# Performance work log

Hardware: AMD Instinct MI355X
Metric: run time of the kernel (lower is better)

Reference implementation:

```python
import jax, jax.numpy as jnp
import numpy as np

N, E, G = 50000, 800000, 64
IN_C, HID, HEADS, OUT_C = 128, 64, 4, 10
NEG_SLOPE = 0.2
EPS = 1e-16


def gat_conv(x, src, dst, W, a_src, a_dst, bias, heads, out_ch):
    # x: [N, F_in]; W: [F_in, heads*out_ch]; a_*: [heads, out_ch]; bias: [heads*out_ch]
    n = x.shape[0]
    h = (x @ W).reshape(n, heads, out_ch)                     # [N, H, C]
    alpha_src = jnp.einsum('nhc,hc->nh', h, a_src)            # [N, H]
    alpha_dst = jnp.einsum('nhc,hc->nh', h, a_dst)            # [N, H]
    e = jax.nn.leaky_relu(alpha_src[src] + alpha_dst[dst], NEG_SLOPE)  # [E, H]
    # segment softmax over incoming edges of each destination node
    m = jax.ops.segment_max(e, dst, num_segments=n)
    ex = jnp.exp(e - m[dst])
    denom = jax.ops.segment_sum(ex, dst, num_segments=n)
    alpha = ex / (denom[dst] + EPS)                           # [E, H]
    msg = h[src] * alpha[:, :, None]                          # [E, H, C]
    out = jax.ops.segment_sum(msg, dst, num_segments=n)       # [N, H, C]
    return out.reshape(n, heads * out_ch) + bias


def setup_inputs() -> dict:
    key = jax.random.key(0)
    ks = jax.random.split(key, 16)
    s = 0.1
    inp = {
        'x': jax.random.normal(ks[0], (N, IN_C), dtype=jnp.float32),
        'edge_index': jax.random.randint(ks[1], (2, E), 0, N, dtype=jnp.int64)
            if jax.config.jax_enable_x64 else jax.random.randint(ks[1], (2, E), 0, N).astype(jnp.int32),
        'batch': jnp.sort(jax.random.randint(ks[2], (N,), 0, G).astype(jnp.int32)),
        'W1': s * jax.random.normal(ks[3], (IN_C, HEADS * HID), dtype=jnp.float32),
        'as1': s * jax.random.normal(ks[4], (HEADS, HID), dtype=jnp.float32),
        'ad1': s * jax.random.normal(ks[5], (HEADS, HID), dtype=jnp.float32),
        'b1': jnp.zeros((HEADS * HID,), jnp.float32),
        'W2': s * jax.random.normal(ks[6], (HEADS * HID, HEADS * HID), dtype=jnp.float32),
        'as2': s * jax.random.normal(ks[7], (HEADS, HID), dtype=jnp.float32),
        'ad2': s * jax.random.normal(ks[8], (HEADS, HID), dtype=jnp.float32),
        'b2': jnp.zeros((HEADS * HID,), jnp.float32),
        'W3': s * jax.random.normal(ks[9], (HEADS * HID, HID), dtype=jnp.float32),
        'as3': s * jax.random.normal(ks[10], (1, HID), dtype=jnp.float32),
        'ad3': s * jax.random.normal(ks[11], (1, HID), dtype=jnp.float32),
        'b3': jnp.zeros((HID,), jnp.float32),
        'Wc': s * jax.random.normal(ks[12], (HID, OUT_C), dtype=jnp.float32),
        'bc': jnp.zeros((OUT_C,), jnp.float32),
    }
    return inp


def reference(x, edge_index, batch, W1, as1, ad1, b1, W2, as2, ad2, b2,
              W3, as3, ad3, b3, Wc, bc):
    n = x.shape[0]
    loop = jnp.arange(n, dtype=edge_index.dtype)
    src = jnp.concatenate([edge_index[0], loop])  # add self-loops (PyG default)
    dst = jnp.concatenate([edge_index[1], loop])

    h = gat_conv(x, src, dst, W1, as1, ad1, b1, HEADS, HID)
    h = jax.nn.elu(h)
    h = gat_conv(h, src, dst, W2, as2, ad2, b2, HEADS, HID)
    h = jax.nn.elu(h)
    h = gat_conv(h, src, dst, W3, as3, ad3, b3, 1, HID)

    # global mean pool over graphs
    sums = jax.ops.segment_sum(h, batch, num_segments=G)            # [G, HID]
    counts = jax.ops.segment_sum(jnp.ones((n,), h.dtype), batch, num_segments=G)
    pooled = sums / jnp.maximum(counts, 1.0)[:, None]

    logits = pooled @ Wc + bc                                       # [G, OUT_C]
    return logits
```

## Files before the change

kernel.cpp:

```cpp
#include <hip/hip_runtime.h>

#define NEG_SLOPE 0.2f
#define EPSV 1e-16f

typedef unsigned short ushort_t;
typedef unsigned char uchar_t;
typedef __attribute__((ext_vector_type(8))) short bf16x8;
typedef __attribute__((ext_vector_type(4))) float f32x4;
typedef __attribute__((ext_vector_type(2))) float f32x2;

__device__ __forceinline__ ushort_t f2bf(float f) {
    union { float f; unsigned u; } v; v.f = f;
    unsigned r = v.u + 0x7FFFu + ((v.u >> 16) & 1u);
    return (ushort_t)(r >> 16);
}
__device__ __forceinline__ float bf2f(ushort_t u) {
    union { unsigned u; float f; } v; v.u = ((unsigned)u) << 16;
    return v.f;
}
__device__ __forceinline__ uchar_t f2fp8(float f) {
    int p = __builtin_amdgcn_cvt_pk_fp8_f32(f, 0.f, 0, false);
    return (uchar_t)(p & 0xff);
}

__global__ __launch_bounds__(256)
void count_kernel(const int* __restrict__ ei, int* __restrict__ deg, int E, int n) {
    int i = blockIdx.x * blockDim.x + threadIdx.x;
    int M = E + n;
    if (i >= M) return;
    int d = (i < E) ? ei[E + i] : (i - E);
    atomicAdd(&deg[d], 1);
}

__global__ __launch_bounds__(1024)
void scan1_kernel(const int* __restrict__ deg, int* __restrict__ indptr,
                  int* __restrict__ bsum, int n) {
    __shared__ int wsum[16];
    const int t = threadIdx.x;
    const int lane = t & 63;
    const int w = t >> 6;
    const int i = blockIdx.x * 1024 + t;
    int v = (i < n) ? deg[i] : 0;
    int s = v;
    #pragma unroll
    for (int off = 1; off < 64; off <<= 1) {
        int u = __shfl_up(s, off);
        if (lane >= off) s += u;
    }
    if (lane == 63) wsum[w] = s;
    __syncthreads();
    if (t < 16) {
        int ws_ = wsum[t];
        #pragma unroll
        for (int off = 1; off < 16; off <<= 1) {
            int u = __shfl_up(ws_, off);
            if (t >= off) ws_ += u;
        }
        wsum[t] = ws_;
    }
    __syncthreads();
    int woff = (w > 0) ? wsum[w - 1] : 0;
    if (i < n) indptr[i + 1] = woff + s;
    if (t == 0) bsum[blockIdx.x] = wsum[15];
}

__global__ __launch_bounds__(1024)
void scan3_kernel(int* __restrict__ indptr, int* __restrict__ cursor,
                  const int* __restrict__ bsum, int nb, int n) {
    __shared__ int boff_s;
    const int t = threadIdx.x;
    if (t < 64) {
        int v = (t < nb) ? bsum[t] : 0;
        int s = v;
        #pragma unroll
        for (int off = 1; off < 64; off <<= 1) {
            int u = __shfl_up(s, off);
            if (t >= off) s += u;
        }
        if (t == (int)blockIdx.x) boff_s = s - v;
    }
    __syncthreads();
    const int boff = boff_s;
    int i = blockIdx.x * 1024 + t;
    if (i < n) {
        int val = indptr[i + 1] + boff;
        indptr[i + 1] = val;
        cursor[i + 1] = val;
    }
    if (i == 0) { indptr[0] = 0; cursor[0] = 0; }
}

__global__ __launch_bounds__(256)
void scatter_kernel(const int* __restrict__ ei, int* __restrict__ cursor,
                    int* __restrict__ csr_src, int E, int n) {
    int i = blockIdx.x * blockDim.x + threadIdx.x;
    int M = E + n;
    if (i >= M) return;
    int s, d;
    if (i < E) { s = ei[i]; d = ei[E + i]; }
    else       { s = i - E; d = i - E; }
    int pos = atomicAdd(&cursor[d], 1);
    csr_src[pos] = s;
}

__global__ __launch_bounds__(256)
void prep_kernel(const float* __restrict__ x, ushort_t* __restrict__ xb, int nx4,
                 const float* __restrict__ W1, ushort_t* __restrict__ Wt1,
                 const float* __restrict__ W2, ushort_t* __restrict__ Wt2,
                 const float* __restrict__ W3, ushort_t* __restrict__ Wt3,
                 int K1, int* __restrict__ deg, int n) {
    long idx = (long)blockIdx.x * 256 + threadIdx.x;
    if (idx < nx4) {
        float4 v = *reinterpret_cast<const float4*>(&x[idx * 4]);
        ushort4 o;
        o.x = f2bf(v.x); o.y = f2bf(v.y); o.z = f2bf(v.z); o.w = f2bf(v.w);
        *reinterpret_cast<ushort4*>(&xb[idx * 4]) = o;
        return;
    }
    idx -= nx4;
    if (idx < (long)K1 * 256) {
        int c = (int)(idx % 256), k = (int)(idx / 256);
        Wt1[(long)c * K1 + k] = f2bf(W1[idx]);
        return;
    }
    idx -= (long)K1 * 256;
    if (idx < 256 * 256) {
        int c = (int)(idx % 256), k = (int)(idx / 256);
        Wt2[(long)c * 256 + k] = f2bf(W2[idx]);
        return;
    }
    idx -= 256 * 256;
    if (idx < 256 * 64) {
        int c = (int)(idx % 64), k = (int)(idx / 64);
        Wt3[(long)c * 256 + k] = f2bf(W3[idx]);
        return;
    }
    idx -= 256 * 64;
    if (idx < n) deg[idx] = 0;
}

template<int NC>
__global__ __launch_bounds__(256)
void mfma_gemm_alpha_kernel(const ushort_t* __restrict__ A, const ushort_t* __restrict__ Wt,
                            uchar_t* __restrict__ C,
                            const float* __restrict__ a_src, const float* __restrict__ a_dst,
                            float* __restrict__ asrc, float* __restrict__ adst,
                            int M, int K, int N, int H) {
    constexpr int TBN = NC * 64;
    constexpr int MI  = (NC == 2) ? 4 : 2;
    __shared__ ushort_t As[128][40];
    __shared__ ushort_t Ws[TBN][40];
    const int tid  = threadIdx.x;
    const int w    = tid >> 6;
    const int lane = tid & 63;
    const int l15  = lane & 15;
    const int l4   = lane >> 4;
    const int row0 = blockIdx.x * 128;
    const int col0 = blockIdx.y * TBN;
    const int rbase = (NC == 2) ? (w & 1) * 64 : w * 32;
    const int cbase = (NC == 2) ? (w >> 1) * 64 : 0;

    f32x4 acc[MI][4];
    #pragma unroll
    for (int mi = 0; mi < MI; ++mi)
        #pragma unroll
        for (int ni = 0; ni < 4; ++ni)
            acc[mi][ni] = (f32x4){0.f, 0.f, 0.f, 0.f};

    for (int k0 = 0; k0 < K; k0 += 32) {
        #pragma unroll
        for (int it = 0; it < 2; ++it) {
            int idx = tid + it * 256;
            int r = idx >> 2, seg = idx & 3;
            int gr = row0 + r;
            uint4 v = make_uint4(0u, 0u, 0u, 0u);
            if (gr < M)
                v = *reinterpret_cast<const uint4*>(&A[(long)gr * K + k0 + seg * 8]);
            *reinterpret_cast<uint4*>(&As[r][seg * 8]) = v;
        }
        #pragma unroll
        for (int it = 0; it < NC; ++it) {
            int idx = tid + it * 256;
            int r = idx >> 2, seg = idx & 3;
            uint4 v = *reinterpret_cast<const uint4*>(&Wt[(long)(col0 + r) * K + k0 + seg * 8]);
            *reinterpret_cast<uint4*>(&Ws[r][seg * 8]) = v;
        }
        __syncthreads();
        bf16x8 af[MI], bfv[4];
        #pragma unroll
        for (int mi = 0; mi < MI; ++mi)
            af[mi] = *reinterpret_cast<const bf16x8*>(&As[rbase + mi * 16 + l15][8 * l4]);
        #pragma unroll
        for (int ni = 0; ni < 4; ++ni)
            bfv[ni] = *reinterpret_cast<const bf16x8*>(&Ws[cbase + ni * 16 + l15][8 * l4]);
        #pragma unroll
        for (int mi = 0; mi < MI; ++mi)
            #pragma unroll
            for (int ni = 0; ni < 4; ++ni)
                acc[mi][ni] = __builtin_amdgcn_mfma_f32_16x16x32_bf16(
                    af[mi], bfv[ni], acc[mi][ni], 0, 0, 0);
        __syncthreads();
    }

    #pragma unroll
    for (int mi = 0; mi < MI; ++mi)
        #pragma unroll
        for (int reg = 0; reg < 4; ++reg) {
            int gr = row0 + rbase + mi * 16 + l4 * 4 + reg;
            if (gr < M) {
                #pragma unroll
                for (int ni = 0; ni < 4; ++ni)
                    C[(long)gr * N + col0 + cbase + ni * 16 + l15] = f2fp8(acc[mi][ni][reg]);
            }
        }

    const int hd = (col0 + cbase) >> 6;
    float aS[4], aD[4];
    #pragma unroll
    for (int ni = 0; ni < 4; ++ni) {
        aS[ni] = a_src[hd * 64 + ni * 16 + l15];
        aD[ni] = a_dst[hd * 64 + ni * 16 + l15];
    }
    #pragma unroll
    for (int mi = 0; mi < MI; ++mi)
        #pragma unroll
        for (int reg = 0; reg < 4; ++reg) {
            float s = 0.f, d = 0.f;
            #pragma unroll
            for (int ni = 0; ni < 4; ++ni) {
                s += acc[mi][ni][reg] * aS[ni];
                d += acc[mi][ni][reg] * aD[ni];
            }
            #pragma unroll
            for (int off = 1; off < 16; off <<= 1) {
                s += __shfl_xor(s, off);
                d += __shfl_xor(d, off);
            }
            int gr = row0 + rbase + mi * 16 + l4 * 4 + reg;
            if (l15 == 0 && gr < M) {
                asrc[gr * H + hd] = s;
                adst[gr * H + hd] = d;
            }
        }
}

__global__ __launch_bounds__(256)
void aggregate4_kernel(const uchar_t* __restrict__ h, const float* __restrict__ asrc,
                       const float* __restrict__ adst, const int* __restrict__ indptr,
                       const int* __restrict__ csr_src, const float* __restrict__ bias,
                       ushort_t* __restrict__ out, int n, int apply_elu) {
    __shared__ int   sOff[4][64];
    __shared__ float sEx[4][4][68];
    const int node = (blockIdx.x * blockDim.x + threadIdx.x) >> 6;
    const int lane = threadIdx.x & 63;
    const int w    = threadIdx.x >> 6;
    if (node >= n) return;
    const int hd   = lane >> 4;
    const int eidx = lane & 15;
    const int beg = indptr[node], end = indptr[node + 1];
    const float ad = adst[node * 4 + hd];
    const uchar_t* __restrict__ hrow = h + 4 * lane;

    float sum_ex = 0.f;
    float ax = 0.f, ay = 0.f, az = 0.f, aw = 0.f;
    for (int cb = beg; cb < end; cb += 64) {
        const int cnt = min(64, end - cb);
        int s[4];
        float ex[4];
        #pragma unroll
        for (int j = 0; j < 4; ++j) {
            int idx = eidx + 16 * j;
            s[j] = (idx < cnt) ? csr_src[cb + idx] : 0;
        }
        #pragma unroll
        for (int j = 0; j < 4; ++j) {
            float t = asrc[s[j] * 4 + hd] + ad;
            t = t > 0.f ? t : NEG_SLOPE * t;
            ex[j] = (eidx + 16 * j < cnt) ? __expf(t) : 0.f;
        }
        float csum = (ex[0] + ex[1]) + (ex[2] + ex[3]);
        #pragma unroll
        for (int off = 1; off < 16; off <<= 1) csum += __shfl_xor(csum, off);
        sum_ex += csum;
        #pragma unroll
        for (int j = 0; j < 4; ++j) sEx[w][hd][eidx + 16 * j] = ex[j];
        if (hd == 0) {
            #pragma unroll
            for (int j = 0; j < 4; ++j) sOff[w][eidx + 16 * j] = s[j] << 8;
        }
        int i = 0;
        for (; i + 8 <= cnt; i += 8) {
            int o[8];
            float ee[8];
            unsigned v[8];
            #pragma unroll
            for (int u = 0; u < 8; ++u) o[u] = sOff[w][i + u];
            #pragma unroll
            for (int u = 0; u < 8; ++u) v[u] = *reinterpret_cast<const unsigned*>(hrow + o[u]);
            #pragma unroll
            for (int u = 0; u < 8; ++u) ee[u] = sEx[w][hd][i + u];
            #pragma unroll
            for (int u = 0; u < 8; ++u) {
                f32x2 lo = __builtin_amdgcn_cvt_pk_f32_fp8((int)v[u], false);
                f32x2 hi = __builtin_amdgcn_cvt_pk_f32_fp8((int)v[u], true);
                ax += ee[u] * lo[0];
                ay += ee[u] * lo[1];
                az += ee[u] * hi[0];
                aw += ee[u] * hi[1];
            }
        }
        for (; i < cnt; ++i) {
            int o = sOff[w][i];
            float ee = sEx[w][hd][i];
            unsigned v = *reinterpret_cast<const unsigned*>(hrow + o);
            f32x2 lo = __builtin_amdgcn_cvt_pk_f32_fp8((int)v, false);
            f32x2 hi = __builtin_amdgcn_cvt_pk_f32_fp8((int)v, true);
            ax += ee * lo[0]; ay += ee * lo[1];
            az += ee * hi[0]; aw += ee * hi[1];
        }
    }
    const float inv = 1.f / (sum_ex + EPSV);
    float4 b4 = *reinterpret_cast<const float4*>(bias + 4 * lane);
    float ox = ax * inv + b4.x;
    float oy = ay * inv + b4.y;
    float oz = az * inv + b4.z;
    float ow = aw * inv + b4.w;
    if (apply_elu) {
        ox = ox > 0.f ? ox : expm1f(ox);
        oy = oy > 0.f ? oy : expm1f(oy);
        oz = oz > 0.f ? oz : expm1f(oz);
        ow = ow > 0.f ? ow : expm1f(ow);
    }
    ushort4 o4;
    o4.x = f2bf(ox); o4.y = f2bf(oy); o4.z = f2bf(oz); o4.w = f2bf(ow);
    *reinterpret_cast<ushort4*>(out + (long)node * 256 + 4 * lane) = o4;
}

__global__ __launch_bounds__(256)
void aggregate_kernel(const uchar_t* __restrict__ h, const float* __restrict__ asrc,
                      const float* __restrict__ adst, const int* __restrict__ indptr,
                      const int* __restrict__ csr_src, const float* __restrict__ bias,
                      ushort_t* __restrict__ out, int n, int apply_elu) {
    __shared__ int   sInd[4][64];
    __shared__ float sEx[4][64];
    const int node = (blockIdx.x * blockDim.x + threadIdx.x) >> 6;
    const int lane = threadIdx.x & 63;
    const int w    = threadIdx.x >> 6;
    if (node >= n) return;
    const int beg = indptr[node];
    const int end = indptr[node + 1];
    const float ad = adst[node];
    const uchar_t* __restrict__ hh = h + lane;

    float sum_ex = 0.f, acc = 0.f;
    for (int cb = beg; cb < end; cb += 64) {
        const int cnt = min(64, end - cb);
        int s = 0;
        float ex = 0.f;
        if (lane < cnt) {
            s = csr_src[cb + lane];
            float e = asrc[s] + ad;
            e = e > 0.f ? e : NEG_SLOPE * e;
            ex = __expf(e);
        }
        float cs = ex;
        #pragma unroll
        for (int off = 32; off > 0; off >>= 1) cs += __shfl_xor(cs, off);
        sum_ex += cs;
        sInd[w][lane] = s;
        sEx[w][lane]  = ex;
        int i = 0;
        for (; i + 8 <= cnt; i += 8) {
            int si[8];
            float ei_[8], vi[8];
            #pragma unroll
            for (int u = 0; u < 8; ++u) si[u] = sInd[w][i + u];
            #pragma unroll
            for (int u = 0; u < 8; ++u) {
                unsigned b = hh[(long)si[u] * 64];
                f32x2 r = __builtin_amdgcn_cvt_pk_f32_fp8((int)b, false);
                vi[u] = r[0];
            }
            #pragma unroll
            for (int u = 0; u < 8; ++u) ei_[u] = sEx[w][i + u];
            #pragma unroll
            for (int u = 0; u < 8; ++u) acc += ei_[u] * vi[u];
        }
        for (; i < cnt; ++i) {
            unsigned b = hh[(long)sInd[w][i] * 64];
            f32x2 r = __builtin_amdgcn_cvt_pk_f32_fp8((int)b, false);
            acc += sEx[w][i] * r[0];
        }
    }
    float o = acc / (sum_ex + EPSV) + bias[lane];
    if (apply_elu) o = o > 0.f ? o : expm1f(o);
    out[(long)node * 64 + lane] = f2bf(o);
}

constexpr int POOL_CHUNK = 128;

__global__ __launch_bounds__(64)
void pool_kernel(const ushort_t* __restrict__ h, const int* __restrict__ batch,
                 float* __restrict__ sums, int* __restrict__ counts, int n) {
    int lane = threadIdx.x;
    int start = blockIdx.x * POOL_CHUNK;
    if (start >= n) return;
    int end = min(start + POOL_CHUNK, n);
    int gcur = batch[start];
    float acc = 0.f;
    int run = 0;
    for (int i = start; i < end; ++i) {
        int g = batch[i];
        if (g != gcur) {
            atomicAdd(&sums[gcur * 64 + lane], acc);
            if (lane == 0) atomicAdd(&counts[gcur], run);
            acc = 0.f; run = 0; gcur = g;
        }
        acc += bf2f(h[(long)i * 64 + lane]);
        ++run;
    }
    atomicAdd(&sums[gcur * 64 + lane], acc);
    if (lane == 0) atomicAdd(&counts[gcur], run);
}

__global__ void classify_kernel(const float* __restrict__ sums, const int* __restrict__ counts,
                                const float* __restrict__ Wc, const float* __restrict__ bc,
                                float* __restrict__ out, int G) {
    int t = threadIdx.x;
    if (t >= G * 10) return;
    int g = t / 10, o = t - g * 10;
    int c_ = counts[g];
    float inv = 1.f / (float)(c_ > 1 ? c_ : 1);
    float acc = bc[o];
    for (int c = 0; c < 64; ++c)
        acc += sums[g * 64 + c] * inv * Wc[c * 10 + o];
    out[t] = acc;
}

extern "C" void kernel_launch(void* const* d_in, const int* in_sizes, int n_in,
                              void* d_out, int out_size, void* d_ws, size_t ws_size,
                              hipStream_t stream) {
    const float* x   = (const float*)d_in[0];
    const int*   ei  = (const int*)d_in[1];
    const int*   bat = (const int*)d_in[2];
    const float* W1  = (const float*)d_in[3];
    const float* as1 = (const float*)d_in[4];
    const float* ad1 = (const float*)d_in[5];
    const float* b1  = (const float*)d_in[6];
    const float* W2  = (const float*)d_in[7];
    const float* as2 = (const float*)d_in[8];
    const float* ad2 = (const float*)d_in[9];
    const float* b2  = (const float*)d_in[10];
    const float* W3  = (const float*)d_in[11];
    const float* as3 = (const float*)d_in[12];
    const float* ad3 = (const float*)d_in[13];
    const float* b3  = (const float*)d_in[14];
    const float* Wc  = (const float*)d_in[15];
    const float* bc  = (const float*)d_in[16];
    float* out = (float*)d_out;

    const int N = in_sizes[2];
    const int E = in_sizes[1] / 2;
    const int M = E + N;
    const int IN_C = in_sizes[0] / N;
    const int G = out_size / 10;

    char* p = (char*)d_ws;
    auto carve = [&](size_t bytes) -> void* {
        void* r = (void*)p;
        p += (bytes + 255) & ~(size_t)255;
        return r;
    };
    uchar_t*  hA  = (uchar_t*)carve((size_t)N * 256);
    ushort_t* hB  = (ushort_t*)carve((size_t)N * 256 * 2);
    ushort_t* xb  = (ushort_t*)carve((size_t)N * IN_C * 2);
    ushort_t* Wt1 = (ushort_t*)carve((size_t)256 * IN_C * 2);
    ushort_t* Wt2 = (ushort_t*)carve((size_t)256 * 256 * 2);
    ushort_t* Wt3 = (ushort_t*)carve((size_t)64 * 256 * 2);
    float* asrc = (float*)carve((size_t)N * 4 * 4);
    float* adst = (float*)carve((size_t)N * 4 * 4);
    float* sums = (float*)carve((size_t)G * 64 * 4 + (size_t)G * 4);
    int*   cnts = (int*)(sums + (size_t)G * 64);
    int*   deg  = (int*)carve((size_t)N * 4);
    int*   iptr = (int*)carve((size_t)(N + 1) * 4);
    int*   csr  = (int*)carve((size_t)M * 4);
    int*   bsum = (int*)carve(256 * 4);
    (void)ws_size; (void)n_in;

    const int NB = (N + 1023) / 1024;

    {
        long nx4 = (long)N * IN_C / 4;
        long total = nx4 + (long)IN_C * 256 + 256 * 256 + 256 * 64 + N;
        prep_kernel<<<(int)((total + 255) / 256), 256, 0, stream>>>(
            x, xb, (int)nx4, W1, Wt1, W2, Wt2, W3, Wt3, IN_C, deg, N);
    }

    count_kernel<<<(M + 255) / 256, 256, 0, stream>>>(ei, deg, E, N);
    scan1_kernel<<<NB, 1024, 0, stream>>>(deg, iptr, bsum, N);
    scan3_kernel<<<NB, 1024, 0, stream>>>(iptr, deg, bsum, NB, N);
    scatter_kernel<<<(M + 255) / 256, 256, 0, stream>>>(ei, deg, csr, E, N);

    {
        dim3 grid((N + 127) / 128, 2);
        mfma_gemm_alpha_kernel<2><<<grid, 256, 0, stream>>>(xb, Wt1, hA, as1, ad1,
                                                            asrc, adst, N, IN_C, 256, 4);
    }
    aggregate4_kernel<<<(N + 3) / 4, 256, 0, stream>>>(hA, asrc, adst, iptr, csr, b1, hB, N, 1);

    {
        dim3 grid((N + 127) / 128, 2);
        mfma_gemm_alpha_kernel<2><<<grid, 256, 0, stream>>>(hB, Wt2, hA, as2, ad2,
                                                            asrc, adst, N, 256, 256, 4);
    }
    aggregate4_kernel<<<(N + 3) / 4, 256, 0, stream>>>(hA, asrc, adst, iptr, csr, b2, hB, N, 1);

    {
        dim3 grid((N + 127) / 128, 1);
        mfma_gemm_alpha_kernel<1><<<grid, 256, 0, stream>>>(hB, Wt3, hA, as3, ad3,
                                                            asrc, adst, N, 256, 64, 1);
    }
    aggregate_kernel<<<(N + 3) / 4, 256, 0, stream>>>(hA, asrc, adst, iptr, csr, b3, hB, N, 0);

    hipMemsetAsync(sums, 0, (size_t)G * 64 * 4 + (size_t)G * 4, stream);
    pool_kernel<<<(N + POOL_CHUNK - 1) / POOL_CHUNK, 64, 0, stream>>>(hB, bat, sums, cnts, N);
    classify_kernel<<<1, 640, 0, stream>>>(sums, cnts, Wc, bc, out, G);
}
```

Before: 448.0 us.

## Precompute per-edge attention exponentials in separate edge-parallel kernels before aggregation

Moves the leaky-relu and exp of the attention logits out of the per-node aggregation kernels into new edge-parallel kernels that write a per-edge ex buffer, using a new CSR destination array produced by scatter. The aggregation kernels drop the LDS staging, the shuffle reductions and the 64-edge chunk loop, and stream csr_src and ex directly from global memory. This removes per-node serial work and shared-memory round trips. In exchange it adds three kernel launches and extra global traffic for the M×16-byte ex buffer, which reuses the xb workspace region.

```diff
diff --git a/kernel.cpp b/kernel.cpp
--- a/kernel.cpp
+++ b/kernel.cpp
@@ -92,7 +92,7 @@
 
 __global__ __launch_bounds__(256)
 void scatter_kernel(const int* __restrict__ ei, int* __restrict__ cursor,
-                    int* __restrict__ csr_src, int E, int n) {
+                    int* __restrict__ csr_src, int* __restrict__ csr_dst, int E, int n) {
     int i = blockIdx.x * blockDim.x + threadIdx.x;
     int M = E + n;
     if (i >= M) return;
@@ -101,6 +101,7 @@
     else       { s = i - E; d = i - E; }
     int pos = atomicAdd(&cursor[d], 1);
     csr_src[pos] = s;
+    csr_dst[pos] = d;
 }
 
 __global__ __launch_bounds__(256)
@@ -245,79 +246,82 @@
 }
 
 __global__ __launch_bounds__(256)
-void aggregate4_kernel(const uchar_t* __restrict__ h, const float* __restrict__ asrc,
-                       const float* __restrict__ adst, const int* __restrict__ indptr,
-                       const int* __restrict__ csr_src, const float* __restrict__ bias,
-                       ushort_t* __restrict__ out, int n, int apply_elu) {
-    __shared__ int   sOff[4][64];
-    __shared__ float sEx[4][4][68];
+void edgeexp4_kernel(const int* __restrict__ csr_src, const int* __restrict__ csr_dst,
+                     const float4* __restrict__ asrc4, const float4* __restrict__ adst4,
+                     float4* __restrict__ ex4, int M) {
+    int i = blockIdx.x * blockDim.x + threadIdx.x;
+    if (i >= M) return;
+    int s = csr_src[i], d = csr_dst[i];
+    float4 a = asrc4[s];
+    float4 b = adst4[d];
+    float ex_, ey_, ez_, ew_;
+    float e;
+    e = a.x + b.x; e = e > 0.f ? e : NEG_SLOPE * e; ex_ = __expf(e);
+    e = a.y + b.y; e = e > 0.f ? e : NEG_SLOPE * e; ey_ = __expf(e);
+    e = a.z + b.z; e = e > 0.f ? e : NEG_SLOPE * e; ez_ = __expf(e);
+    e = a.w + b.w; e = e > 0.f ? e : NEG_SLOPE * e; ew_ = __expf(e);
+    ex4[i] = make_float4(ex_, ey_, ez_, ew_);
+}
+
+__global__ __launch_bounds__(256)
+void edgeexp1_kernel(const int* __restrict__ csr_src, const int* __restrict__ csr_dst,
+                     const float* __restrict__ asrc, const float* __restrict__ adst,
+                     float* __restrict__ ex1, int M) {
+    int i = blockIdx.x * blockDim.x + threadIdx.x;
+    if (i >= M) return;
+    float e = asrc[csr_src[i]] + adst[csr_dst[i]];
+    e = e > 0.f ? e : NEG_SLOPE * e;
+    ex1[i] = __expf(e);
+}
+
+__global__ __launch_bounds__(256)
+void aggregate4_kernel(const uchar_t* __restrict__ h, const float* __restrict__ ex4,
+                       const int* __restrict__ indptr, const int* __restrict__ csr_src,
+                       const float* __restrict__ bias, ushort_t* __restrict__ out,
+                       int n, int apply_elu) {
     const int node = (blockIdx.x * blockDim.x + threadIdx.x) >> 6;
     const int lane = threadIdx.x & 63;
-    const int w    = threadIdx.x >> 6;
     if (node >= n) return;
-    const int hd   = lane >> 4;
-    const int eidx = lane & 15;
+    const int hd  = lane >> 4;
     const int beg = indptr[node], end = indptr[node + 1];
-    const float ad = adst[node * 4 + hd];
+    const int cnt = end - beg;
     const uchar_t* __restrict__ hrow = h + 4 * lane;
+    const float* __restrict__ exh = ex4 + 4 * (long)beg + hd;
 
     float sum_ex = 0.f;
     float ax = 0.f, ay = 0.f, az = 0.f, aw = 0.f;
-    for (int cb = beg; cb < end; cb += 64) {
-        const int cnt = min(64, end - cb);
-        int s[4];
-        float ex[4];
-        #pragma unroll
-        for (int j = 0; j < 4; ++j) {
-            int idx = eidx + 16 * j;
-            s[j] = (idx < cnt) ? csr_src[cb + idx] : 0;
-        }
-        #pragma unroll
-        for (int j = 0; j < 4; ++j) {
-            float t = asrc[s[j] * 4 + hd] + ad;
-            t = t > 0.f ? t : NEG_SLOPE * t;
-            ex[j] = (eidx + 16 * j < cnt) ? __expf(t) : 0.f;
-        }
-        float csum = (ex[0] + ex[1]) + (ex[2] + ex[3]);
-        #pragma unroll
-        for (int off = 1; off < 16; off <<= 1) csum += __shfl_xor(csum, off);
-        sum_ex += csum;
-        #pragma unroll
-        for (int j = 0; j < 4; ++j) sEx[w][hd][eidx + 16 * j] = ex[j];
-        if (hd == 0) {
-            #pragma unroll
-            for (int j = 0; j < 4; ++j) sOff[w][eidx + 16 * j] = s[j] << 8;
-        }
-        int i = 0;
-        for (; i + 8 <= cnt; i += 8) {
-            int o[8];
-            float ee[8];
-            unsigned v[8];
-            #pragma unroll
-            for (int u = 0; u < 8; ++u) o[u] = sOff[w][i + u];
-            #pragma unroll
-            for (int u = 0; u < 8; ++u) v[u] = *reinterpret_cast<const unsigned*>(hrow + o[u]);
-            #pragma unroll
-            for (int u = 0; u < 8; ++u) ee[u] = sEx[w][hd][i + u];
-            #pragma unroll
-            for (int u = 0; u < 8; ++u) {
-                f32x2 lo = __builtin_amdgcn_cvt_pk_f32_fp8((int)v[u], false);
-                f32x2 hi = __builtin_amdgcn_cvt_pk_f32_fp8((int)v[u], true);
-                ax += ee[u] * lo[0];
-                ay += ee[u] * lo[1];
-                az += ee[u] * hi[0];
-                aw += ee[u] * hi[1];
-            }
-        }
-        for (; i < cnt; ++i) {
-            int o = sOff[w][i];
-            float ee = sEx[w][hd][i];
-            unsigned v = *reinterpret_cast<const unsigned*>(hrow + o);
-            f32x2 lo = __builtin_amdgcn_cvt_pk_f32_fp8((int)v, false);
-            f32x2 hi = __builtin_amdgcn_cvt_pk_f32_fp8((int)v, true);
-            ax += ee * lo[0]; ay += ee * lo[1];
-            az += ee * hi[0]; aw += ee * hi[1];
-        }
+    int i = 0;
+    for (; i + 8 <= cnt; i += 8) {
+        int s[8];
+        float ee[8];
+        unsigned v[8];
+        #pragma unroll
+        for (int u = 0; u < 8; ++u) s[u] = csr_src[beg + i + u];
+        #pragma unroll
+        for (int u = 0; u < 8; ++u) ee[u] = exh[(long)(i + u) * 4];
+        #pragma unroll
+        for (int u = 0; u < 8; ++u)
+            v[u] = *reinterpret_cast<const unsigned*>(hrow + ((long)s[u] << 8));
+        #pragma unroll
+        for (int u = 0; u < 8; ++u) {
+            f32x2 lo = __builtin_amdgcn_cvt_pk_f32_fp8((int)v[u], false);
+            f32x2 hi = __builtin_amdgcn_cvt_pk_f32_fp8((int)v[u], true);
+            sum_ex += ee[u];
+            ax += ee[u] * lo[0];
+            ay += ee[u] * lo[1];
+            az += ee[u] * hi[0];
+            aw += ee[u] * hi[1];
+        }
+    }
+    for (; i < cnt; ++i) {
+        int s = csr_src[beg + i];
+        float ee = exh[(long)i * 4];
+        unsigned v = *reinterpret_cast<const unsigned*>(hrow + ((long)s << 8));
+        f32x2 lo = __builtin_amdgcn_cvt_pk_f32_fp8((int)v, false);
+        f32x2 hi = __builtin_amdgcn_cvt_pk_f32_fp8((int)v, true);
+        sum_ex += ee;
+        ax += ee * lo[0]; ay += ee * lo[1];
+        az += ee * hi[0]; aw += ee * hi[1];
     }
     const float inv = 1.f / (sum_ex + EPSV);
     float4 b4 = *reinterpret_cast<const float4*>(bias + 4 * lane);
@@ -337,60 +341,42 @@
 }
 
 __global__ __launch_bounds__(256)
-void aggregate_kernel(const uchar_t* __restrict__ h, const float* __restrict__ asrc,
-                      const float* __restrict__ adst, const int* __restrict__ indptr,
-                      const int* __restrict__ csr_src, const float* __restrict__ bias,
-                      ushort_t* __restrict__ out, int n, int apply_elu) {
-    __shared__ int   sInd[4][64];
-    __shared__ float sEx[4][64];
+void aggregate_kernel(const uchar_t* __restrict__ h, const float* __restrict__ ex1,
+                      const int* __restrict__ indptr, const int* __restrict__ csr_src,
+                      const float* __restrict__ bias, ushort_t* __restrict__ out,
+                      int n, int apply_elu) {
     const int node = (blockIdx.x * blockDim.x + threadIdx.x) >> 6;
     const int lane = threadIdx.x & 63;
-    const int w    = threadIdx.x >> 6;
     if (node >= n) return;
-    const int beg = indptr[node];
-    const int end = indptr[node + 1];
-    const float ad = adst[node];
+    const int beg = indptr[node], end = indptr[node + 1];
+    const int cnt = end - beg;
     const uchar_t* __restrict__ hh = h + lane;
 
     float sum_ex = 0.f, acc = 0.f;
-    for (int cb = beg; cb < end; cb += 64) {
-        const int cnt = min(64, end - cb);
-        int s = 0;
-        float ex = 0.f;
-        if (lane < cnt) {
-            s = csr_src[cb + lane];
-            float e = asrc[s] + ad;
-            e = e > 0.f ? e : NEG_SLOPE * e;
-            ex = __expf(e);
-        }
-        float cs = ex;
-        #pragma unroll
-        for (int off = 32; off > 0; off >>= 1) cs += __shfl_xor(cs, off);
-        sum_ex += cs;
-        sInd[w][lane] = s;
-        sEx[w][lane]  = ex;
-        int i = 0;
-        for (; i + 8 <= cnt; i += 8) {
-            int si[8];
-            float ei_[8], vi[8];
-            #pragma unroll
-            for (int u = 0; u < 8; ++u) si[u] = sInd[w][i + u];
-            #pragma unroll
-            for (int u = 0; u < 8; ++u) {
-                unsigned b = hh[(long)si[u] * 64];
-                f32x2 r = __builtin_amdgcn_cvt_pk_f32_fp8((int)b, false);
-                vi[u] = r[0];
-            }
-            #pragma unroll
-            for (int u = 0; u < 8; ++u) ei_[u] = sEx[w][i + u];
-            #pragma unroll
-            for (int u = 0; u < 8; ++u) acc += ei_[u] * vi[u];
-        }
-        for (; i < cnt; ++i) {
-            unsigned b = hh[(long)sInd[w][i] * 64];
-            f32x2 r = __builtin_amdgcn_cvt_pk_f32_fp8((int)b, false);
-            acc += sEx[w][i] * r[0];
-        }
+    int i = 0;
+    for (; i + 8 <= cnt; i += 8) {
+        int s[8];
+        float ee[8];
+        uchar_t b[8];
+        #pragma unroll
+        for (int u = 0; u < 8; ++u) s[u] = csr_src[beg + i + u];
+        #pragma unroll
+        for (int u = 0; u < 8; ++u) ee[u] = ex1[beg + i + u];
+        #pragma unroll
+        for (int u = 0; u < 8; ++u) b[u] = hh[(long)s[u] << 6];
+        #pragma unroll
+        for (int u = 0; u < 8; ++u) {
+            f32x2 r = __builtin_amdgcn_cvt_pk_f32_fp8((int)b[u], false);
+            sum_ex += ee[u];
+            acc += ee[u] * r[0];
+        }
+    }
+    for (; i < cnt; ++i) {
+        int s = csr_src[beg + i];
+        float ee = ex1[beg + i];
+        f32x2 r = __builtin_amdgcn_cvt_pk_f32_fp8((int)hh[(long)s << 6], false);
+        sum_ex += ee;
+        acc += ee * r[0];
     }
     float o = acc / (sum_ex + EPSV) + bias[lane];
     if (apply_elu) o = o > 0.f ? o : expm1f(o);
@@ -473,7 +459,11 @@
     };
     uchar_t*  hA  = (uchar_t*)carve((size_t)N * 256);
     ushort_t* hB  = (ushort_t*)carve((size_t)N * 256 * 2);
-    ushort_t* xb  = (ushort_t*)carve((size_t)N * IN_C * 2);
+    size_t xb_ex_bytes = (size_t)M * 16;
+    size_t xb_need = (size_t)N * IN_C * 2;
+    if (xb_need > xb_ex_bytes) xb_ex_bytes = xb_need;
+    ushort_t* xb  = (ushort_t*)carve(xb_ex_bytes);
+    float*    ex  = (float*)xb;
     ushort_t* Wt1 = (ushort_t*)carve((size_t)256 * IN_C * 2);
     ushort_t* Wt2 = (ushort_t*)carve((size_t)256 * 256 * 2);
     ushort_t* Wt3 = (ushort_t*)carve((size_t)64 * 256 * 2);
@@ -484,10 +474,13 @@
     int*   deg  = (int*)carve((size_t)N * 4);
     int*   iptr = (int*)carve((size_t)(N + 1) * 4);
     int*   csr  = (int*)carve((size_t)M * 4);
+    int*   csrd = (int*)carve((size_t)M * 4);
     int*   bsum = (int*)carve(256 * 4);
     (void)ws_size; (void)n_in;
 
     const int NB = (N + 1023) / 1024;
+    const int MB = (M + 255) / 256;
+    const int AGB = (N + 3) / 4;
 
     {
         long nx4 = (long)N * IN_C / 4;
@@ -496,31 +489,36 @@
             x, xb, (int)nx4, W1, Wt1, W2, Wt2, W3, Wt3, IN_C, deg, N);
     }
 
-    count_kernel<<<(M + 255) / 256, 256, 0, stream>>>(ei, deg, E, N);
+    count_kernel<<<MB, 256, 0, stream>>>(ei, deg, E, N);
     scan1_kernel<<<NB, 1024, 0, stream>>>(deg, iptr, bsum, N);
     scan3_kernel<<<NB, 1024, 0, stream>>>(iptr, deg, bsum, NB, N);
-    scatter_kernel<<<(M + 255) / 256, 256, 0, stream>>>(ei, deg, csr, E, N);
+    scatter_kernel<<<MB, 256, 0, stream>>>(ei, deg, csr, csrd, E, N);
 
     {
         dim3 grid((N + 127) / 128, 2);
         mfma_gemm_alpha_kernel<2><<<grid, 256, 0, stream>>>(xb, Wt1, hA, as1, ad1,
                                                             asrc, adst, N, IN_C, 256, 4);
     }
-    aggregate4_kernel<<<(N + 3) / 4, 256, 0, stream>>>(hA, asrc, adst, iptr, csr, b1, hB, N, 1);
+    edgeexp4_kernel<<<MB, 256, 0, stream>>>(csr, csrd, (const float4*)asrc,
+                                            (const float4*)adst, (float4*)ex, M);
+    aggregate4_kernel<<<AGB, 256, 0, stream>>>(hA, ex, iptr, csr, b1, hB, N, 1);
 
     {
         dim3 grid((N + 127) / 128, 2);
         mfma_gemm_alpha_kernel<2><<<grid, 256, 0, stream>>>(hB, Wt2, hA, as2, ad2,
                                                             asrc, adst, N, 256, 256, 4);
     }
-    aggregate4_kernel<<<(N + 3) / 4, 256, 0, stream>>>(hA, asrc, adst, iptr, csr, b2, hB, N, 1);
+    edgeexp4_kernel<<<MB, 256, 0, stream>>>(csr, csrd, (const float4*)asrc,
+                                            (const float4*)adst, (float4*)ex, M);
+    aggregate4_kernel<<<AGB, 256, 0, stream>>>(hA, ex, iptr, csr, b2, hB, N, 1);
 
     {
         dim3 grid((N + 127) / 128, 1);
         mfma_gemm_alpha_kernel<1><<<grid, 256, 0, stream>>>(hB, Wt3, hA, as3, ad3,
                                                             asrc, adst, N, 256, 64, 1);
     }
-    aggregate_kernel<<<(N + 3) / 4, 256, 0, stream>>>(hA, asrc, adst, iptr, csr, b3, hB, N, 0);
+    edgeexp1_kernel<<<MB, 256, 0, stream>>>(csr, csrd, asrc, adst, ex, M);
+    aggregate_kernel<<<AGB, 256, 0, stream>>>(hA, ex, iptr, csr, b3, hB, N, 0);
 
     hipMemsetAsync(sums, 0, (size_t)G * 64 * 4 + (size_t)G * 4, stream);
     pool_kernel<<<(N + POOL_CHUNK - 1) / POOL_CHUNK, 64, 0, stream>>>(hB, bat, sums, cnts, N);
```

After: 454.2 us. About the same (+1.4%).
